# Kernel optimization log

Hardware: AMD Instinct MI355X
Metric: run time of the kernel (lower is better)

Reference implementation:

```python
import jax, jax.numpy as jnp
import numpy as np

B, S, E, H = 2, 2048, 1024, 16
HD = E // H


def setup_inputs() -> dict:
    key = jax.random.key(0)
    k1, k2, k3, k4 = jax.random.split(key, 4)
    x = jax.random.normal(k1, (B, S, E), dtype=jnp.float32)
    # nn.Linear(E, 3E, bias=False): weight shape (3E, E), y = x @ W.T
    w_qkv = jax.random.normal(k2, (3 * E, E), dtype=jnp.float32) * (E ** -0.5)
    w_proj = jax.random.normal(k3, (E, E), dtype=jnp.float32) * (E ** -0.5)
    b_proj = jax.random.normal(k4, (E,), dtype=jnp.float32) * 0.02
    return {"x": x, "w_qkv": w_qkv, "w_proj": w_proj, "b_proj": b_proj}


def reference(x, w_qkv, w_proj, b_proj):
    b, s, e = x.shape
    hd = e // H
    qkv = x @ w_qkv.T                                   # (B,S,3E)
    qkv = qkv.reshape(b, s, H, 3, hd)                   # matches view(B,S,H,3*hd).chunk(3,-1)
    q = jnp.transpose(qkv[..., 0, :], (0, 2, 1, 3))      # (B,H,S,hd)
    k = jnp.transpose(qkv[..., 1, :], (0, 2, 1, 3))
    v = jnp.transpose(qkv[..., 2, :], (0, 2, 1, 3))
    scale = hd ** -0.5
    scores = jnp.einsum('bhqd,bhkd->bhqk', q, k) * scale  # (B,H,S,S)
    causal = jnp.tril(jnp.ones((s, s), dtype=bool))
    scores = jnp.where(causal, scores, jnp.float32(-jnp.inf))
    probs = jax.nn.softmax(scores, axis=-1)
    out = jnp.einsum('bhqk,bhkd->bhqd', probs, v)        # (B,H,S,hd)
    out = jnp.transpose(out, (0, 2, 1, 3)).reshape(b, s, e)
    return out @ w_proj.T + b_proj
```

## Files before the change

kernel.cpp:

```cpp
#include <hip/hip_runtime.h>
#include <hip/hip_bf16.h>

#define B_    2
#define S_    2048
#define E_    1024
#define H_    16
#define HD_   64
#define M_    (B_ * S_)
#define QKVN  (3 * E_)

typedef __attribute__((ext_vector_type(8))) short  short8;
typedef __attribute__((ext_vector_type(4))) float  f32x4;
typedef __attribute__((ext_vector_type(4))) unsigned short us16x4;

static __device__ __forceinline__ unsigned short f2bf(float f) {
  union { float f; unsigned int u; } c; c.f = f;
  unsigned int u = c.u;
  return (unsigned short)((u + 0x7fffu + ((u >> 16) & 1u)) >> 16);
}

static __device__ __forceinline__ void gload16(unsigned short* lds,
                                               const unsigned short* g) {
  __builtin_amdgcn_global_load_lds(
      (__attribute__((address_space(1))) void*)g,
      (__attribute__((address_space(3))) void*)lds, 16, 0, 0);
}

__global__ __launch_bounds__(256) void cvt_f32_to_bf16(
    const float* __restrict__ in, unsigned short* __restrict__ out, int n4) {
  int i = blockIdx.x * 256 + threadIdx.x;
  if (i < n4) {
    float4 v = reinterpret_cast<const float4*>(in)[i];
    ushort4 r;
    r.x = f2bf(v.x); r.y = f2bf(v.y); r.z = f2bf(v.z); r.w = f2bf(v.w);
    reinterpret_cast<ushort4*>(out)[i] = r;
  }
}

template <int BF16_OUT>
__global__ __launch_bounds__(256) void gemm_bt(
    const unsigned short* __restrict__ A, const unsigned short* __restrict__ Bt,
    void* __restrict__ Cout, const float* __restrict__ bias,
    int M, int N, int K, int ldc) {
  __shared__ alignas(16) unsigned short lds_a[128 * 64];
  __shared__ alignas(16) unsigned short lds_b[128 * 64];
  const int t  = threadIdx.x;
  const int w  = t >> 6, l = t & 63, g = l >> 4, lr = l & 15;
  const int bm = blockIdx.y * 128, bn = blockIdx.x * 128;
  const int wr = (w >> 1) * 64,  wc = (w & 1) * 64;

  f32x4 acc[4][4] = {};

  for (int k0 = 0; k0 < K; k0 += 64) {
    __syncthreads();
#pragma unroll
    for (int i = 0; i < 4; i++) {
      const int pass = w * 4 + i;
      const int r = pass * 8 + (l >> 3);
      const int c = (l & 7) ^ (r & 7);
      gload16(lds_a + pass * 512, A + (size_t)(bm + r) * K + k0 + c * 8);
      gload16(lds_b + pass * 512, Bt + (size_t)(bn + r) * K + k0 + c * 8);
    }
    __syncthreads();

    short8 af[4][2], bfr[4][2];
#pragma unroll
    for (int m = 0; m < 4; m++) {
      const int R = wr + m * 16 + lr;
#pragma unroll
      for (int kk = 0; kk < 2; kk++)
        af[m][kk] = *(const short8*)((const char*)lds_a +
            ((R * 128 + kk * 64 + g * 16) ^ ((R & 7) << 4)));
    }
#pragma unroll
    for (int n = 0; n < 4; n++) {
      const int R = wc + n * 16 + lr;
#pragma unroll
      for (int kk = 0; kk < 2; kk++)
        bfr[n][kk] = *(const short8*)((const char*)lds_b +
            ((R * 128 + kk * 64 + g * 16) ^ ((R & 7) << 4)));
    }
#pragma unroll
    for (int m = 0; m < 4; m++)
#pragma unroll
      for (int n = 0; n < 4; n++) {
        acc[m][n] = __builtin_amdgcn_mfma_f32_16x16x32_bf16(
            af[m][0], bfr[n][0], acc[m][n], 0, 0, 0);
        acc[m][n] = __builtin_amdgcn_mfma_f32_16x16x32_bf16(
            af[m][1], bfr[n][1], acc[m][n], 0, 0, 0);
      }
  }

#pragma unroll
  for (int m = 0; m < 4; m++)
#pragma unroll
    for (int n = 0; n < 4; n++)
#pragma unroll
      for (int j = 0; j < 4; j++) {
        const int row = bm + wr + m * 16 + g * 4 + j;
        const int col = bn + wc + n * 16 + lr;
        const float v = acc[m][n][j];
        if constexpr (BF16_OUT) {
          ((unsigned short*)Cout)[(size_t)row * ldc + col] = f2bf(v);
        } else {
          ((float*)Cout)[(size_t)row * ldc + col] = v + bias[col];
        }
      }
}

__global__ __launch_bounds__(256) void attn_fwd(
    const unsigned short* __restrict__ qkv, unsigned short* __restrict__ attn_out) {
  __shared__ alignas(16) unsigned short lds_k[64 * 64];
  __shared__ alignas(16) unsigned short lds_vt[64 * 64];
  __shared__ alignas(16) unsigned short lds_p[4][32 * 64];

  const int t = threadIdx.x;
  const int w = t >> 6, l = t & 63, g = (l >> 4) & 3, lr = l & 15;
  const int bid = blockIdx.x;
  const int bh = bid & 31, b = bh >> 4, h = bh & 15;
  const int rr = bid >> 5;
  const int bx = (rr < 8) ? rr : 23 - rr;
  const int q0 = bx * 128;
  const int qw = q0 + w * 32;
  const unsigned short* base = qkv + (size_t)b * S_ * QKVN + h * (3 * HD_);

  short8 qf[2][2];
#pragma unroll
  for (int m = 0; m < 2; m++) {
    const unsigned short* qp = base + (size_t)(qw + m * 16 + lr) * QKVN + g * 8;
    qf[m][0] = *(const short8*)qp;
    qf[m][1] = *(const short8*)(qp + 32);
  }

  f32x4 o[2][4] = {};
  float m_r[2] = {-3.0e38f, -3.0e38f};
  float l_r[2] = {0.f, 0.f};
  const float SCALE2 = 0.18033688011112042f;

  const int numt = 2 * bx + 2;
  const int r_st = t >> 3;
  const int kc   = t & 7;

  short8 kreg[2], vreg[2];
#pragma unroll
  for (int p = 0; p < 2; p++) {
    const unsigned short* kp =
        base + (size_t)(p * 32 + r_st) * QKVN + HD_ + kc * 8;
    kreg[p] = *(const short8*)kp;
    vreg[p] = *(const short8*)(kp + HD_);
  }

  for (int kt = 0; kt < numt; kt++) {
    const int k0 = kt * 64;
#pragma unroll
    for (int p = 0; p < 2; p++) {
      const int r = p * 32 + r_st;
      *(short8*)((char*)lds_k + ((r * 128 + kc * 16) ^ ((r & 7) << 4))) = kreg[p];
#pragma unroll
      for (int j = 0; j < 8; j++) {
        const int d = kc * 8 + j;
        const int swz = ((d & 7) ^ ((d >> 3) & 7)) << 4;
        *(unsigned short*)((char*)lds_vt + ((d * 128 + r * 2) ^ swz)) =
            (unsigned short)vreg[p][j];
      }
    }
    if (kt + 1 < numt) {
#pragma unroll
      for (int p = 0; p < 2; p++) {
        const unsigned short* kp =
            base + (size_t)(k0 + 64 + p * 32 + r_st) * QKVN + HD_ + kc * 8;
        kreg[p] = *(const short8*)kp;
        vreg[p] = *(const short8*)(kp + HD_);
      }
    }
    __syncthreads();

    if (k0 <= qw + 31) {
      f32x4 st[2][4];
      __builtin_amdgcn_s_setprio(1);
#pragma unroll
      for (int n = 0; n < 4; n++) {
        const int R = n * 16 + lr;
        const int sw = (R & 7) << 4;
        short8 kf0 = *(const short8*)((const char*)lds_k +
            ((R * 128 + g * 16) ^ sw));
        short8 kf1 = *(const short8*)((const char*)lds_k +
            ((R * 128 + 64 + g * 16) ^ sw));
#pragma unroll
        for (int m = 0; m < 2; m++) {
          f32x4 z = {};
          z = __builtin_amdgcn_mfma_f32_16x16x32_bf16(kf0, qf[m][0], z, 0, 0, 0);
          z = __builtin_amdgcn_mfma_f32_16x16x32_bf16(kf1, qf[m][1], z, 0, 0, 0);
          st[m][n] = z;
        }
      }
      __builtin_amdgcn_s_setprio(0);

      const bool diag = (k0 + 63 > qw);

#pragma unroll
      for (int m = 0; m < 2; m++) {
        const int qrow = qw + m * 16 + lr;
        if (diag) {
#pragma unroll
          for (int n = 0; n < 4; n++)
#pragma unroll
            for (int j = 0; j < 4; j++)
              if ((k0 + n * 16 + g * 4 + j) > qrow) st[m][n][j] = -3.0e38f;
        }
        float mx = st[m][0][0];
#pragma unroll
        for (int n = 0; n < 4; n++)
#pragma unroll
          for (int j = 0; j < 4; j++) mx = fmaxf(mx, st[m][n][j]);
        mx = fmaxf(mx, __shfl_xor(mx, 16, 64));
        mx = fmaxf(mx, __shfl_xor(mx, 32, 64));
        const float mn = fmaxf(m_r[m], mx * SCALE2);
        const float c  = exp2f(m_r[m] - mn);
        m_r[m] = mn;
        float p[4][4];
        float sum = 0.f;
#pragma unroll
        for (int n = 0; n < 4; n++)
#pragma unroll
          for (int j = 0; j < 4; j++) {
            p[n][j] = exp2f(fmaf(st[m][n][j], SCALE2, -mn));
            sum += p[n][j];
          }
        sum += __shfl_xor(sum, 16, 64);
        sum += __shfl_xor(sum, 32, 64);
        l_r[m] = l_r[m] * c + sum;
#pragma unroll
        for (int dt = 0; dt < 4; dt++) o[m][dt] *= c;
        char* pb = (char*)lds_p[w];
        const int rowb = (m * 16 + lr) * 128;
        const int sw   = (lr & 7) << 4;
#pragma unroll
        for (int n = 0; n < 4; n++) {
          unsigned w0, w1;
          __asm__("v_cvt_pk_bf16_f32 %0, %1, %2"
                  : "=v"(w0) : "v"(p[n][0]), "v"(p[n][1]));
          __asm__("v_cvt_pk_bf16_f32 %0, %1, %2"
                  : "=v"(w1) : "v"(p[n][2]), "v"(p[n][3]));
          uint2 val; val.x = w0; val.y = w1;
          *(uint2*)(pb + ((rowb + n * 32 + g * 8) ^ sw)) = val;
        }
      }
      __asm__ volatile("s_waitcnt lgkmcnt(0)" ::: "memory");

      short8 pf[2][2];
#pragma unroll
      for (int m = 0; m < 2; m++) {
        const int rowb = (m * 16 + lr) * 128;
        const int sw   = (lr & 7) << 4;
        pf[m][0] = *(const short8*)((const char*)lds_p[w] +
            ((rowb + g * 16) ^ sw));
        pf[m][1] = *(const short8*)((const char*)lds_p[w] +
            ((rowb + 64 + g * 16) ^ sw));
      }
      __builtin_amdgcn_s_setprio(1);
#pragma unroll
      for (int dt = 0; dt < 4; dt++) {
        const int R = dt * 16 + lr;
        const int vsw = ((R & 7) ^ ((R >> 3) & 7)) << 4;
        short8 vf0 = *(const short8*)((const char*)lds_vt +
            ((R * 128 + g * 16) ^ vsw));
        short8 vf1 = *(const short8*)((const char*)lds_vt +
            ((R * 128 + 64 + g * 16) ^ vsw));
#pragma unroll
        for (int m = 0; m < 2; m++) {
          o[m][dt] = __builtin_amdgcn_mfma_f32_16x16x32_bf16(
              vf0, pf[m][0], o[m][dt], 0, 0, 0);
          o[m][dt] = __builtin_amdgcn_mfma_f32_16x16x32_bf16(
              vf1, pf[m][1], o[m][dt], 0, 0, 0);
        }
      }
      __builtin_amdgcn_s_setprio(0);
    }

    __syncthreads();
  }

  unsigned short* outp = attn_out + (size_t)b * S_ * E_ + h * HD_;
#pragma unroll
  for (int m = 0; m < 2; m++) {
    const float inv = 1.0f / l_r[m];
    const int qrow = qw + m * 16 + lr;
#pragma unroll
    for (int dt = 0; dt < 4; dt++) {
      us16x4 w4;
#pragma unroll
      for (int j = 0; j < 4; j++) w4[j] = f2bf(o[m][dt][j] * inv);
      *(us16x4*)(outp + (size_t)qrow * E_ + dt * 16 + g * 4) = w4;
    }
  }
}

extern "C" void kernel_launch(void* const* d_in, const int* in_sizes, int n_in,
                              void* d_out, int out_size, void* d_ws, size_t ws_size,
                              hipStream_t stream) {
  (void)in_sizes; (void)n_in; (void)out_size; (void)ws_size;
  const float* x      = (const float*)d_in[0];
  const float* w_qkv  = (const float*)d_in[1];
  const float* w_proj = (const float*)d_in[2];
  const float* b_proj = (const float*)d_in[3];
  float* out = (float*)d_out;

  unsigned short* x_bf     = (unsigned short*)d_ws;
  unsigned short* wqkv_bf  = x_bf    + (size_t)M_ * E_;
  unsigned short* wproj_bf = wqkv_bf + (size_t)QKVN * E_;
  unsigned short* qkv_bf   = wproj_bf + (size_t)E_ * E_;
  unsigned short* attn_bf  = qkv_bf  + (size_t)M_ * QKVN;

  int n4;
  n4 = M_ * E_ / 4;
  cvt_f32_to_bf16<<<(n4 + 255) / 256, 256, 0, stream>>>(x, x_bf, n4);
  n4 = QKVN * E_ / 4;
  cvt_f32_to_bf16<<<(n4 + 255) / 256, 256, 0, stream>>>(w_qkv, wqkv_bf, n4);
  n4 = E_ * E_ / 4;
  cvt_f32_to_bf16<<<(n4 + 255) / 256, 256, 0, stream>>>(w_proj, wproj_bf, n4);

  gemm_bt<1><<<dim3(QKVN / 128, M_ / 128), 256, 0, stream>>>(
      x_bf, wqkv_bf, (void*)qkv_bf, nullptr, M_, QKVN, E_, QKVN);

  attn_fwd<<<dim3(512), 256, 0, stream>>>(qkv_bf, attn_bf);

  gemm_bt<0><<<dim3(E_ / 128, M_ / 128), 256, 0, stream>>>(
      attn_bf, wproj_bf, (void*)out, b_proj, M_, E_, E_, E_);
}
```

Measured before the change: 213.2 us.

## Write Q, K and transposed V separately from QKV GEMM; narrow projection tiles

The QKV GEMM epilogue now scatters its output into separate Q, K and pre-transposed V buffers. This lets the attention kernel store V into LDS with a single vector write instead of eight scalar transposing writes per row. The output projection GEMM is templated on tile width and launched with 64-column tiles, doubling its grid to fill more CUs. The cost is an uncoalesced strided V^T store in the GEMM epilogue and lower per-block reuse in the projection GEMM.

```diff
diff --git a/kernel.cpp b/kernel.cpp
--- a/kernel.cpp
+++ b/kernel.cpp
@@ -37,19 +37,20 @@
   }
 }
 
-template <int BF16_OUT>
+template <int BF16_OUT, int BN>
 __global__ __launch_bounds__(256) void gemm_bt(
     const unsigned short* __restrict__ A, const unsigned short* __restrict__ Bt,
     void* __restrict__ Cout, const float* __restrict__ bias,
     int M, int N, int K, int ldc) {
+  constexpr int NF = BN / 32;
   __shared__ alignas(16) unsigned short lds_a[128 * 64];
-  __shared__ alignas(16) unsigned short lds_b[128 * 64];
+  __shared__ alignas(16) unsigned short lds_b[BN * 64];
   const int t  = threadIdx.x;
   const int w  = t >> 6, l = t & 63, g = l >> 4, lr = l & 15;
-  const int bm = blockIdx.y * 128, bn = blockIdx.x * 128;
-  const int wr = (w >> 1) * 64,  wc = (w & 1) * 64;
-
-  f32x4 acc[4][4] = {};
+  const int bm = blockIdx.y * 128, bn = blockIdx.x * BN;
+  const int wr = (w >> 1) * 64,  wc = (w & 1) * (BN / 2);
+
+  f32x4 acc[4][NF] = {};
 
   for (int k0 = 0; k0 < K; k0 += 64) {
     __syncthreads();
@@ -59,11 +60,17 @@
       const int r = pass * 8 + (l >> 3);
       const int c = (l & 7) ^ (r & 7);
       gload16(lds_a + pass * 512, A + (size_t)(bm + r) * K + k0 + c * 8);
+    }
+#pragma unroll
+    for (int i = 0; i < NF; i++) {
+      const int pass = w * NF + i;
+      const int r = pass * 8 + (l >> 3);
+      const int c = (l & 7) ^ (r & 7);
       gload16(lds_b + pass * 512, Bt + (size_t)(bn + r) * K + k0 + c * 8);
     }
     __syncthreads();
 
-    short8 af[4][2], bfr[4][2];
+    short8 af[4][2], bfr[NF][2];
 #pragma unroll
     for (int m = 0; m < 4; m++) {
       const int R = wr + m * 16 + lr;
@@ -73,7 +80,7 @@
             ((R * 128 + kk * 64 + g * 16) ^ ((R & 7) << 4)));
     }
 #pragma unroll
-    for (int n = 0; n < 4; n++) {
+    for (int n = 0; n < NF; n++) {
       const int R = wc + n * 16 + lr;
 #pragma unroll
       for (int kk = 0; kk < 2; kk++)
@@ -83,7 +90,7 @@
 #pragma unroll
     for (int m = 0; m < 4; m++)
 #pragma unroll
-      for (int n = 0; n < 4; n++) {
+      for (int n = 0; n < NF; n++) {
         acc[m][n] = __builtin_amdgcn_mfma_f32_16x16x32_bf16(
             af[m][0], bfr[n][0], acc[m][n], 0, 0, 0);
         acc[m][n] = __builtin_amdgcn_mfma_f32_16x16x32_bf16(
@@ -94,7 +101,7 @@
 #pragma unroll
   for (int m = 0; m < 4; m++)
 #pragma unroll
-    for (int n = 0; n < 4; n++)
+    for (int n = 0; n < NF; n++)
 #pragma unroll
       for (int j = 0; j < 4; j++) {
         const int row = bm + wr + m * 16 + g * 4 + j;
@@ -108,8 +115,96 @@
       }
 }
 
+__global__ __launch_bounds__(256) void gemm_qkv(
+    const unsigned short* __restrict__ A, const unsigned short* __restrict__ Bt,
+    unsigned short* __restrict__ q_bf, unsigned short* __restrict__ k_bf,
+    unsigned short* __restrict__ vt_bf, int K) {
+  __shared__ alignas(16) unsigned short lds_a[128 * 64];
+  __shared__ alignas(16) unsigned short lds_b[128 * 64];
+  const int t  = threadIdx.x;
+  const int w  = t >> 6, l = t & 63, g = l >> 4, lr = l & 15;
+  const int bm = blockIdx.y * 128, bn = blockIdx.x * 128;
+  const int wr = (w >> 1) * 64,  wc = (w & 1) * 64;
+
+  f32x4 acc[4][4] = {};
+
+  for (int k0 = 0; k0 < K; k0 += 64) {
+    __syncthreads();
+#pragma unroll
+    for (int i = 0; i < 4; i++) {
+      const int pass = w * 4 + i;
+      const int r = pass * 8 + (l >> 3);
+      const int c = (l & 7) ^ (r & 7);
+      gload16(lds_a + pass * 512, A + (size_t)(bm + r) * K + k0 + c * 8);
+      gload16(lds_b + pass * 512, Bt + (size_t)(bn + r) * K + k0 + c * 8);
+    }
+    __syncthreads();
+
+    short8 af[4][2], bfr[4][2];
+#pragma unroll
+    for (int m = 0; m < 4; m++) {
+      const int R = wr + m * 16 + lr;
+#pragma unroll
+      for (int kk = 0; kk < 2; kk++)
+        af[m][kk] = *(const short8*)((const char*)lds_a +
+            ((R * 128 + kk * 64 + g * 16) ^ ((R & 7) << 4)));
+    }
+#pragma unroll
+    for (int n = 0; n < 4; n++) {
+      const int R = wc + n * 16 + lr;
+#pragma unroll
+      for (int kk = 0; kk < 2; kk++)
+        bfr[n][kk] = *(const short8*)((const char*)lds_b +
+            ((R * 128 + kk * 64 + g * 16) ^ ((R & 7) << 4)));
+    }
+#pragma unroll
+    for (int m = 0; m < 4; m++)
+#pragma unroll
+      for (int n = 0; n < 4; n++) {
+        acc[m][n] = __builtin_amdgcn_mfma_f32_16x16x32_bf16(
+            af[m][0], bfr[n][0], acc[m][n], 0, 0, 0);
+        acc[m][n] = __builtin_amdgcn_mfma_f32_16x16x32_bf16(
+            af[m][1], bfr[n][1], acc[m][n], 0, 0, 0);
+      }
+  }
+
+  const int b = bm >> 11;
+#pragma unroll
+  for (int n = 0; n < 4; n++) {
+    const int col0  = bn + wc + n * 16;
+    const int hcls  = col0 / 192;
+    const int cls   = (col0 % 192) / 64;
+    const int cbase = col0 & 63;
+    if (cls == 2) {
+      const int d  = cbase + lr;
+      const int sl = (bm & 2047) + wr + g * 4;
+#pragma unroll
+      for (int m = 0; m < 4; m++) {
+        us16x4 pk;
+#pragma unroll
+        for (int j = 0; j < 4; j++) pk[j] = f2bf(acc[m][n][j]);
+        *(us16x4*)(vt_bf +
+            ((size_t)((b * H_ + hcls) * 64 + d) * S_ + sl + m * 16)) = pk;
+      }
+    } else {
+      unsigned short* dst = (cls == 0) ? q_bf : k_bf;
+      const int col = hcls * 64 + cbase + lr;
+#pragma unroll
+      for (int m = 0; m < 4; m++)
+#pragma unroll
+        for (int j = 0; j < 4; j++) {
+          const int row = bm + wr + m * 16 + g * 4 + j;
+          dst[(size_t)row * E_ + col] = f2bf(acc[m][n][j]);
+        }
+    }
+  }
+}
+
 __global__ __launch_bounds__(256) void attn_fwd(
-    const unsigned short* __restrict__ qkv, unsigned short* __restrict__ attn_out) {
+    const unsigned short* __restrict__ q_bf,
+    const unsigned short* __restrict__ k_bf,
+    const unsigned short* __restrict__ vt_bf,
+    unsigned short* __restrict__ attn_out) {
   __shared__ alignas(16) unsigned short lds_k[64 * 64];
   __shared__ alignas(16) unsigned short lds_vt[64 * 64];
   __shared__ alignas(16) unsigned short lds_p[4][32 * 64];
@@ -122,12 +217,14 @@
   const int bx = (rr < 8) ? rr : 23 - rr;
   const int q0 = bx * 128;
   const int qw = q0 + w * 32;
-  const unsigned short* base = qkv + (size_t)b * S_ * QKVN + h * (3 * HD_);
+  const unsigned short* qbase = q_bf + (size_t)b * S_ * E_ + h * HD_;
+  const unsigned short* kbase = k_bf + (size_t)b * S_ * E_ + h * HD_;
+  const unsigned short* vbase = vt_bf + (size_t)(b * H_ + h) * 64 * S_;
 
   short8 qf[2][2];
 #pragma unroll
   for (int m = 0; m < 2; m++) {
-    const unsigned short* qp = base + (size_t)(qw + m * 16 + lr) * QKVN + g * 8;
+    const unsigned short* qp = qbase + (size_t)(qw + m * 16 + lr) * E_ + g * 8;
     qf[m][0] = *(const short8*)qp;
     qf[m][1] = *(const short8*)(qp + 32);
   }
@@ -144,10 +241,9 @@
   short8 kreg[2], vreg[2];
 #pragma unroll
   for (int p = 0; p < 2; p++) {
-    const unsigned short* kp =
-        base + (size_t)(p * 32 + r_st) * QKVN + HD_ + kc * 8;
-    kreg[p] = *(const short8*)kp;
-    vreg[p] = *(const short8*)(kp + HD_);
+    const int r = p * 32 + r_st;
+    kreg[p] = *(const short8*)(kbase + (size_t)r * E_ + kc * 8);
+    vreg[p] = *(const short8*)(vbase + (size_t)r * S_ + kc * 8);
   }
 
   for (int kt = 0; kt < numt; kt++) {
@@ -155,22 +251,16 @@
 #pragma unroll
     for (int p = 0; p < 2; p++) {
       const int r = p * 32 + r_st;
-      *(short8*)((char*)lds_k + ((r * 128 + kc * 16) ^ ((r & 7) << 4))) = kreg[p];
-#pragma unroll
-      for (int j = 0; j < 8; j++) {
-        const int d = kc * 8 + j;
-        const int swz = ((d & 7) ^ ((d >> 3) & 7)) << 4;
-        *(unsigned short*)((char*)lds_vt + ((d * 128 + r * 2) ^ swz)) =
-            (unsigned short)vreg[p][j];
-      }
+      const int off = (r * 128 + kc * 16) ^ ((r & 7) << 4);
+      *(short8*)((char*)lds_k + off)  = kreg[p];
+      *(short8*)((char*)lds_vt + off) = vreg[p];
     }
     if (kt + 1 < numt) {
 #pragma unroll
       for (int p = 0; p < 2; p++) {
-        const unsigned short* kp =
-            base + (size_t)(k0 + 64 + p * 32 + r_st) * QKVN + HD_ + kc * 8;
-        kreg[p] = *(const short8*)kp;
-        vreg[p] = *(const short8*)(kp + HD_);
+        const int r = p * 32 + r_st;
+        kreg[p] = *(const short8*)(kbase + (size_t)(k0 + 64 + r) * E_ + kc * 8);
+        vreg[p] = *(const short8*)(vbase + (size_t)r * S_ + k0 + 64 + kc * 8);
       }
     }
     __syncthreads();
@@ -262,11 +352,11 @@
 #pragma unroll
       for (int dt = 0; dt < 4; dt++) {
         const int R = dt * 16 + lr;
-        const int vsw = ((R & 7) ^ ((R >> 3) & 7)) << 4;
+        const int sw = (R & 7) << 4;
         short8 vf0 = *(const short8*)((const char*)lds_vt +
-            ((R * 128 + g * 16) ^ vsw));
+            ((R * 128 + g * 16) ^ sw));
         short8 vf1 = *(const short8*)((const char*)lds_vt +
-            ((R * 128 + 64 + g * 16) ^ vsw));
+            ((R * 128 + 64 + g * 16) ^ sw));
 #pragma unroll
         for (int m = 0; m < 2; m++) {
           o[m][dt] = __builtin_amdgcn_mfma_f32_16x16x32_bf16(
@@ -309,8 +399,10 @@
   unsigned short* x_bf     = (unsigned short*)d_ws;
   unsigned short* wqkv_bf  = x_bf    + (size_t)M_ * E_;
   unsigned short* wproj_bf = wqkv_bf + (size_t)QKVN * E_;
-  unsigned short* qkv_bf   = wproj_bf + (size_t)E_ * E_;
-  unsigned short* attn_bf  = qkv_bf  + (size_t)M_ * QKVN;
+  unsigned short* q_bf     = wproj_bf + (size_t)E_ * E_;
+  unsigned short* k_bf     = q_bf    + (size_t)M_ * E_;
+  unsigned short* vt_bf    = k_bf    + (size_t)M_ * E_;
+  unsigned short* attn_bf  = vt_bf   + (size_t)M_ * E_;
 
   int n4;
   n4 = M_ * E_ / 4;
@@ -320,11 +412,11 @@
   n4 = E_ * E_ / 4;
   cvt_f32_to_bf16<<<(n4 + 255) / 256, 256, 0, stream>>>(w_proj, wproj_bf, n4);
 
-  gemm_bt<1><<<dim3(QKVN / 128, M_ / 128), 256, 0, stream>>>(
-      x_bf, wqkv_bf, (void*)qkv_bf, nullptr, M_, QKVN, E_, QKVN);
-
-  attn_fwd<<<dim3(512), 256, 0, stream>>>(qkv_bf, attn_bf);
-
-  gemm_bt<0><<<dim3(E_ / 128, M_ / 128), 256, 0, stream>>>(
+  gemm_qkv<<<dim3(QKVN / 128, M_ / 128), 256, 0, stream>>>(
+      x_bf, wqkv_bf, q_bf, k_bf, vt_bf, E_);
+
+  attn_fwd<<<dim3(512), 256, 0, stream>>>(q_bf, k_bf, vt_bf, attn_bf);
+
+  gemm_bt<0, 64><<<dim3(E_ / 64, M_ / 128), 256, 0, stream>>>(
       attn_bf, wproj_bf, (void*)out, b_proj, M_, E_, E_, E_);
 }
```

New measurement: 215.4 us. Within noise of the previous version (+1.0%).
